# Performance work log

Hardware: AMD Instinct MI355X
Metric: run time of the kernel (lower is better)

The kernel has to match this reference:

```python
import jax, jax.numpy as jnp
import numpy as np

B, D, H = 16384, 64, 128
L = D - 1  # number of per-dimension sub-networks (layers 1..dim-1)
W_SCALE = 0.05  # keep alpha outputs small so exp(alpha) stays well-conditioned


def setup_inputs() -> dict:
    key = jax.random.key(0)
    ks = jax.random.split(key, 8)
    return {
        "x": jax.random.normal(ks[0], (B, D), dtype=jnp.float32),
        "W1": jax.random.normal(ks[1], (L, D - 1, H), dtype=jnp.float32) * W_SCALE,
        "b1": jax.random.normal(ks[2], (L, H), dtype=jnp.float32) * W_SCALE,
        "W2": jax.random.normal(ks[3], (L, H, H), dtype=jnp.float32) * W_SCALE,
        "b2": jax.random.normal(ks[4], (L, H), dtype=jnp.float32) * W_SCALE,
        "W3": jax.random.normal(ks[5], (L, H, 2), dtype=jnp.float32) * W_SCALE,
        "b3": jax.random.normal(ks[6], (L, 2), dtype=jnp.float32) * W_SCALE,
        "initial_param": jax.random.uniform(
            ks[7], (2,), dtype=jnp.float32,
            minval=-np.sqrt(0.5), maxval=np.sqrt(0.5)),
    }


def reference(x, W1, b1, W2, b2, W3, b3, initial_param):
    # x: [B, D]. Layer l (l=0..L-1) corresponds to dim i=l+1 and consumes
    # x[:, :l+1]; we realize the ragged inputs via a triangular mask on W1.
    b, d = x.shape
    # mask[l, j] = 1 if input feature j is visible to layer l (j <= l)
    mask = (jnp.arange(d - 1)[None, :] <= jnp.arange(L)[:, None]).astype(x.dtype)
    W1m = W1 * mask[:, :, None]                       # [L, D-1, H]
    h = jnp.tanh(jnp.einsum('bd,ldh->blh', x[:, :d - 1], W1m) + b1)  # [B, L, H]
    h = jnp.tanh(jnp.einsum('blh,lhk->blk', h, W2) + b2)             # [B, L, H]
    out = jnp.einsum('blh,lho->blo', h, W3) + b3                     # [B, L, 2]
    mu0 = jnp.broadcast_to(initial_param[0], (b, 1))
    a0 = jnp.broadcast_to(initial_param[1], (b, 1))
    mu = jnp.concatenate([mu0, out[..., 0]], axis=1)   # [B, D]
    alpha = jnp.concatenate([a0, out[..., 1]], axis=1)  # [B, D]
    z = (x - mu) * jnp.exp(-alpha)
    log_det = -jnp.sum(alpha, axis=1)                  # [B]
    return z[:, ::-1], log_det
```

## Files before the change

### kernel.cpp

```cpp
#include <hip/hip_runtime.h>
#include <hip/hip_bf16.h>
#include <stdint.h>

#define B_N   16384
#define L_N   63
#define K2LOG2E 2.8853900817779268f
#define LOG2E   1.4426950408889634f

typedef unsigned int   u32;
typedef unsigned short u16;
typedef __attribute__((ext_vector_type(8))) __bf16 bf16x8;
typedef __attribute__((ext_vector_type(4))) float  f32x4;

__device__ __forceinline__ u16 f2b(float f){
  u32 u = __builtin_bit_cast(u32, f);
  u += 0x7fffu + ((u >> 16) & 1u);
  return (u16)(u >> 16);
}
__device__ __forceinline__ u32 pk_bf16(float lo, float hi){
  u32 r;
  asm("v_cvt_pk_bf16_f32 %0, %1, %2" : "=v"(r) : "v"(lo), "v"(hi));
  return r;
}
__device__ __forceinline__ float tanh_pre(float a){
  float t = __builtin_amdgcn_exp2f(a * K2LOG2E);
  float r = __builtin_amdgcn_rcpf(t + 1.0f);
  return fmaf(-2.0f, r, 1.0f);
}
__device__ __forceinline__ float tanh_b(float acc, float bb){
  float t = __builtin_amdgcn_exp2f(fmaf(acc, K2LOG2E, bb));
  float r = __builtin_amdgcn_rcpf(t + 1.0f);
  return fmaf(-2.0f, r, 1.0f);
}

__global__ void k_conv_w(const float* __restrict__ W1, const float* __restrict__ b1,
                         const float* __restrict__ W2,
                         u16* __restrict__ w1t, u16* __restrict__ w2t){
  __shared__ u16 t[16384];
  const int l = blockIdx.x, tid = threadIdx.x;
  #pragma unroll
  for (int i = 0; i < 32; ++i) t[i*256 + tid] = 0;
  __syncthreads();
  for (int i = 0; i < 32; ++i){
    int idx = i*256 + tid;
    if (idx < 63*128){
      int d = idx >> 7, n = idx & 127;
      if (d <= l) t[n*64 + d] = f2b(W1[(l*63 + d)*128 + n]);
    }
  }
  if (tid < 128) t[tid*64 + 63] = f2b(b1[l*128 + tid]);
  __syncthreads();
  {
    uint4* o = (uint4*)(w1t + l*(128*64));
    const uint4* s4 = (const uint4*)t;
    #pragma unroll
    for (int i = 0; i < 4; ++i) o[i*256 + tid] = s4[i*256 + tid];
  }
  __syncthreads();
  #pragma unroll
  for (int i = 0; i < 64; ++i){
    int idx = i*256 + tid;
    int h = idx >> 7, n = idx & 127;
    t[n*128 + h] = f2b(W2[l*16384 + idx]);
  }
  __syncthreads();
  {
    uint4* o = (uint4*)(w2t + l*(128*128));
    const uint4* s4 = (const uint4*)t;
    #pragma unroll
    for (int i = 0; i < 8; ++i) o[i*256 + tid] = s4[i*256 + tid];
  }
}

__global__ void k_conv_x(const float* __restrict__ x, u16* __restrict__ out){
  int idx = blockIdx.x*256 + threadIdx.x;
  float4 v = ((const float4*)x)[idx];
  ushort4 r;
  r.x = f2b(v.x); r.y = f2b(v.y); r.z = f2b(v.z);
  r.w = ((idx & 15) == 15) ? (u16)0x3F80 : f2b(v.w);
  ((ushort4*)out)[idx] = r;
}

__global__ __launch_bounds__(256, 4)
void k_main(const u16* __restrict__ W1T, const u16* __restrict__ W2T,
            const u16* __restrict__ xbf, const float* __restrict__ x,
            const float* __restrict__ b2, const float* __restrict__ W3,
            const float* __restrict__ b3,
            float* __restrict__ out, float* __restrict__ alph)
{
  __shared__ __align__(16) u16 h1[128*128];
  __shared__ float2 sc[4][128];
  const int tid = threadIdx.x;
  const int l  = blockIdx.y;
  const int bx = blockIdx.x;
  const int wv = tid >> 6;
  const int ln = tid & 63;
  const int c  = ln & 15;
  const int g  = ln >> 4;
  const int rowbase = bx*128;
  const int sx = (c & 7) << 4;
  char* const h1b = (char*)h1;

  const u16* w1p = W1T + l*(128*64);
  const u16* w2p = W2T + l*(128*128);

  bf16x8 a1f[2][2];
  #pragma unroll
  for (int m = 0; m < 2; ++m)
    #pragma unroll
    for (int s = 0; s < 2; ++s)
      a1f[m][s] = *(const bf16x8*)(w1p + ((2*wv+m)*16 + c)*64 + s*32 + g*8);

  f32x4 acc[2][8] = {};
  #pragma unroll
  for (int s = 0; s < 2; ++s)
    #pragma unroll
    for (int bt = 0; bt < 8; ++bt){
      bf16x8 xf = *(const bf16x8*)(xbf + (size_t)(rowbase + bt*16 + c)*64 + s*32 + g*8);
      acc[0][bt] = __builtin_amdgcn_mfma_f32_16x16x32_bf16(a1f[0][s], xf, acc[0][bt], 0,0,0);
      acc[1][bt] = __builtin_amdgcn_mfma_f32_16x16x32_bf16(a1f[1][s], xf, acc[1][bt], 0,0,0);
    }

  #pragma unroll
  for (int m = 0; m < 2; ++m){
    int h0 = (2*wv+m)*16 + g*4;
    #pragma unroll
    for (int bt = 0; bt < 8; ++bt){
      u32 p0 = pk_bf16(tanh_pre(acc[m][bt][0]), tanh_pre(acc[m][bt][1]));
      u32 p1 = pk_bf16(tanh_pre(acc[m][bt][2]), tanh_pre(acc[m][bt][3]));
      int b = bt*16 + c;
      *(uint2*)(h1b + b*256 + ((h0*2) ^ sx)) = make_uint2(p0, p1);
    }
  }
  __syncthreads();

  f32x4 acc2[2][8] = {};
  #pragma unroll
  for (int s = 0; s < 4; ++s){
    bf16x8 a0 = *(const bf16x8*)(w2p + ((2*wv+0)*16 + c)*128 + s*32 + g*8);
    bf16x8 a1 = *(const bf16x8*)(w2p + ((2*wv+1)*16 + c)*128 + s*32 + g*8);
    #pragma unroll
    for (int bt = 0; bt < 8; ++bt){
      int b = bt*16 + c;
      bf16x8 hf = *(const bf16x8*)(h1b + b*256 + ((s*64 + g*16) ^ sx));
      acc2[0][bt] = __builtin_amdgcn_mfma_f32_16x16x32_bf16(a0, hf, acc2[0][bt], 0,0,0);
      acc2[1][bt] = __builtin_amdgcn_mfma_f32_16x16x32_bf16(a1, hf, acc2[1][bt], 0,0,0);
    }
  }

  float part[8][2] = {};
  #pragma unroll
  for (int m = 0; m < 2; ++m){
    int q = (2*wv+m)*4 + g;
    float4 bbv = ((const float4*)(b2 + l*128))[q];
    float4 w3a = ((const float4*)(W3 + l*256))[q*2 + 0];
    float4 w3b = ((const float4*)(W3 + l*256))[q*2 + 1];
    float bb[4]  = { bbv.x*K2LOG2E, bbv.y*K2LOG2E, bbv.z*K2LOG2E, bbv.w*K2LOG2E };
    float w30[4] = { w3a.x, w3a.z, w3b.x, w3b.z };
    float w31[4] = { w3a.y, w3a.w, w3b.y, w3b.w };
    #pragma unroll
    for (int bt = 0; bt < 8; ++bt)
      #pragma unroll
      for (int r = 0; r < 4; ++r){
        float h2 = tanh_b(acc2[m][bt][r], bb[r]);
        part[bt][0] = fmaf(h2, w30[r], part[bt][0]);
        part[bt][1] = fmaf(h2, w31[r], part[bt][1]);
      }
  }
  #pragma unroll
  for (int bt = 0; bt < 8; ++bt)
    #pragma unroll
    for (int o = 0; o < 2; ++o){
      float v = part[bt][o];
      v += __shfl_xor(v, 16, 64);
      v += __shfl_xor(v, 32, 64);
      part[bt][o] = v;
    }
  if (g == 0){
    #pragma unroll
    for (int bt = 0; bt < 8; ++bt)
      sc[wv][bt*16 + c] = make_float2(part[bt][0], part[bt][1]);
  }
  __syncthreads();

  if (tid < 128){
    int row = rowbase + tid;
    float2 s0 = sc[0][tid], s1 = sc[1][tid], s2 = sc[2][tid], s3 = sc[3][tid];
    float muv = s0.x + s1.x + s2.x + s3.x + b3[l*2 + 0];
    float alv = s0.y + s1.y + s2.y + s3.y + b3[l*2 + 1];
    float xv  = x[(size_t)row*64 + l + 1];
    out[(size_t)row*64 + 62 - l] = (xv - muv) * __builtin_amdgcn_exp2f(-alv * LOG2E);
    alph[(size_t)row*64 + l + 1] = alv;
  }
}

__global__ void k_fin(const float* __restrict__ x, const float* __restrict__ alph,
                      const float* __restrict__ ip, float* __restrict__ out)
{
  int row = blockIdx.x*4 + (threadIdx.x >> 6);
  int d   = threadIdx.x & 63;
  float a = (d == 0) ? ip[1] : alph[(size_t)row*64 + d];
  float s = a;
  #pragma unroll
  for (int off = 32; off; off >>= 1) s += __shfl_xor(s, off, 64);
  if (d == 0){
    out[(size_t)row*64 + 63] = (x[(size_t)row*64] - ip[0]) * __builtin_amdgcn_exp2f(-a * LOG2E);
    out[(size_t)B_N*64 + row] = -s;
  }
}

extern "C" void kernel_launch(void* const* d_in, const int* in_sizes, int n_in,
                              void* d_out, int out_size, void* d_ws, size_t ws_size,
                              hipStream_t stream)
{
  const float* x  = (const float*)d_in[0];
  const float* W1 = (const float*)d_in[1];
  const float* b1 = (const float*)d_in[2];
  const float* W2 = (const float*)d_in[3];
  const float* b2 = (const float*)d_in[4];
  const float* W3 = (const float*)d_in[5];
  const float* b3 = (const float*)d_in[6];
  const float* ip = (const float*)d_in[7];

  char* ws = (char*)d_ws;
  u16*   w1t  = (u16*)(ws);
  u16*   w2t  = (u16*)(ws + 1048576);
  u16*   xbf  = (u16*)(ws + 3145728);
  float* alph = (float*)(ws + 5242880);
  if (ws_size < 9437184) return;

  k_conv_w<<<L_N, 256, 0, stream>>>(W1, b1, W2, w1t, w2t);
  k_conv_x<<<(B_N*64/4)/256, 256, 0, stream>>>(x, xbf);

  dim3 grid(B_N/128, L_N);
  k_main<<<grid, 256, 0, stream>>>(w1t, w2t, xbf, x, b2, W3, b3,
                                   (float*)d_out, alph);

  k_fin<<<B_N/4, 256, 0, stream>>>(x, alph, ip, (float*)d_out);
}
```

Before: 149.4 us.

## Split main kernel work by batch rows per wave, removing block barriers

Each wave now owns 32 batch rows and computes all 128 hidden units for them, instead of each wave owning 32 hidden units across all 128 rows. The first-layer output stays in a private LDS region per wave, so both __syncthreads and the cross-wave reduction through shared memory go away, and each wave writes its own mu/alpha results. In exchange, every wave loads the full W1 and W2 tiles from global/L2, about four times the weight traffic per block, and the row-level output stores are now spread over lanes with g==0 across waves.

After: 240.9 us. +61.3%, slower.

```diff
diff --git a/kernel.cpp b/kernel.cpp
--- a/kernel.cpp
+++ b/kernel.cpp
@@ -88,8 +88,7 @@
             const float* __restrict__ b3,
             float* __restrict__ out, float* __restrict__ alph)
 {
-  __shared__ __align__(16) u16 h1[128*128];
-  __shared__ float2 sc[4][128];
+  __shared__ __align__(16) char lds[32768];
   const int tid = threadIdx.x;
   const int l  = blockIdx.y;
   const int bx = blockIdx.x;
@@ -97,61 +96,60 @@
   const int ln = tid & 63;
   const int c  = ln & 15;
   const int g  = ln >> 4;
-  const int rowbase = bx*128;
+  const int row0 = bx*128 + wv*32;
+  char* const my = lds + wv*8192;
   const int sx = (c & 7) << 4;
-  char* const h1b = (char*)h1;
 
   const u16* w1p = W1T + l*(128*64);
   const u16* w2p = W2T + l*(128*128);
 
-  bf16x8 a1f[2][2];
-  #pragma unroll
-  for (int m = 0; m < 2; ++m)
+  bf16x8 xf[2][2];
+  #pragma unroll
+  for (int bt = 0; bt < 2; ++bt)
     #pragma unroll
     for (int s = 0; s < 2; ++s)
-      a1f[m][s] = *(const bf16x8*)(w1p + ((2*wv+m)*16 + c)*64 + s*32 + g*8);
-
-  f32x4 acc[2][8] = {};
-  #pragma unroll
-  for (int s = 0; s < 2; ++s)
-    #pragma unroll
-    for (int bt = 0; bt < 8; ++bt){
-      bf16x8 xf = *(const bf16x8*)(xbf + (size_t)(rowbase + bt*16 + c)*64 + s*32 + g*8);
-      acc[0][bt] = __builtin_amdgcn_mfma_f32_16x16x32_bf16(a1f[0][s], xf, acc[0][bt], 0,0,0);
-      acc[1][bt] = __builtin_amdgcn_mfma_f32_16x16x32_bf16(a1f[1][s], xf, acc[1][bt], 0,0,0);
-    }
-
-  #pragma unroll
-  for (int m = 0; m < 2; ++m){
-    int h0 = (2*wv+m)*16 + g*4;
-    #pragma unroll
-    for (int bt = 0; bt < 8; ++bt){
-      u32 p0 = pk_bf16(tanh_pre(acc[m][bt][0]), tanh_pre(acc[m][bt][1]));
-      u32 p1 = pk_bf16(tanh_pre(acc[m][bt][2]), tanh_pre(acc[m][bt][3]));
+      xf[bt][s] = *(const bf16x8*)(xbf + (size_t)(row0 + bt*16 + c)*64 + s*32 + g*8);
+
+  #pragma unroll
+  for (int m = 0; m < 8; ++m){
+    const u16* ap = w1p + (m*16 + c)*64 + g*8;
+    bf16x8 a0 = *(const bf16x8*)(ap);
+    bf16x8 a1 = *(const bf16x8*)(ap + 32);
+    f32x4 acc[2] = {};
+    acc[0] = __builtin_amdgcn_mfma_f32_16x16x32_bf16(a0, xf[0][0], acc[0], 0,0,0);
+    acc[0] = __builtin_amdgcn_mfma_f32_16x16x32_bf16(a1, xf[0][1], acc[0], 0,0,0);
+    acc[1] = __builtin_amdgcn_mfma_f32_16x16x32_bf16(a0, xf[1][0], acc[1], 0,0,0);
+    acc[1] = __builtin_amdgcn_mfma_f32_16x16x32_bf16(a1, xf[1][1], acc[1], 0,0,0);
+    #pragma unroll
+    for (int bt = 0; bt < 2; ++bt){
+      u32 p0 = pk_bf16(tanh_pre(acc[bt][0]), tanh_pre(acc[bt][1]));
+      u32 p1 = pk_bf16(tanh_pre(acc[bt][2]), tanh_pre(acc[bt][3]));
       int b = bt*16 + c;
-      *(uint2*)(h1b + b*256 + ((h0*2) ^ sx)) = make_uint2(p0, p1);
-    }
-  }
-  __syncthreads();
-
-  f32x4 acc2[2][8] = {};
-  #pragma unroll
-  for (int s = 0; s < 4; ++s){
-    bf16x8 a0 = *(const bf16x8*)(w2p + ((2*wv+0)*16 + c)*128 + s*32 + g*8);
-    bf16x8 a1 = *(const bf16x8*)(w2p + ((2*wv+1)*16 + c)*128 + s*32 + g*8);
-    #pragma unroll
-    for (int bt = 0; bt < 8; ++bt){
+      *(uint2*)(my + b*256 + ((m*32 + g*8) ^ sx)) = make_uint2(p0, p1);
+    }
+  }
+
+  bf16x8 hf[4][2];
+  #pragma unroll
+  for (int s = 0; s < 4; ++s)
+    #pragma unroll
+    for (int bt = 0; bt < 2; ++bt){
       int b = bt*16 + c;
-      bf16x8 hf = *(const bf16x8*)(h1b + b*256 + ((s*64 + g*16) ^ sx));
-      acc2[0][bt] = __builtin_amdgcn_mfma_f32_16x16x32_bf16(a0, hf, acc2[0][bt], 0,0,0);
-      acc2[1][bt] = __builtin_amdgcn_mfma_f32_16x16x32_bf16(a1, hf, acc2[1][bt], 0,0,0);
-    }
-  }
-
-  float part[8][2] = {};
-  #pragma unroll
-  for (int m = 0; m < 2; ++m){
-    int q = (2*wv+m)*4 + g;
+      hf[s][bt] = *(const bf16x8*)(my + b*256 + ((s*64 + g*16) ^ sx));
+    }
+
+  float part[2][2] = {};
+  #pragma unroll
+  for (int m = 0; m < 8; ++m){
+    const u16* ap = w2p + (m*16 + c)*128 + g*8;
+    f32x4 acc[2] = {};
+    #pragma unroll
+    for (int s = 0; s < 4; ++s){
+      bf16x8 a = *(const bf16x8*)(ap + s*32);
+      acc[0] = __builtin_amdgcn_mfma_f32_16x16x32_bf16(a, hf[s][0], acc[0], 0,0,0);
+      acc[1] = __builtin_amdgcn_mfma_f32_16x16x32_bf16(a, hf[s][1], acc[1], 0,0,0);
+    }
+    int q = m*4 + g;
     float4 bbv = ((const float4*)(b2 + l*128))[q];
     float4 w3a = ((const float4*)(W3 + l*256))[q*2 + 0];
     float4 w3b = ((const float4*)(W3 + l*256))[q*2 + 1];
@@ -159,16 +157,17 @@
     float w30[4] = { w3a.x, w3a.z, w3b.x, w3b.z };
     float w31[4] = { w3a.y, w3a.w, w3b.y, w3b.w };
     #pragma unroll
-    for (int bt = 0; bt < 8; ++bt)
+    for (int bt = 0; bt < 2; ++bt)
       #pragma unroll
       for (int r = 0; r < 4; ++r){
-        float h2 = tanh_b(acc2[m][bt][r], bb[r]);
+        float h2 = tanh_b(acc[bt][r], bb[r]);
         part[bt][0] = fmaf(h2, w30[r], part[bt][0]);
         part[bt][1] = fmaf(h2, w31[r], part[bt][1]);
       }
   }
-  #pragma unroll
-  for (int bt = 0; bt < 8; ++bt)
+
+  #pragma unroll
+  for (int bt = 0; bt < 2; ++bt)
     #pragma unroll
     for (int o = 0; o < 2; ++o){
       float v = part[bt][o];
@@ -178,19 +177,14 @@
     }
   if (g == 0){
     #pragma unroll
-    for (int bt = 0; bt < 8; ++bt)
-      sc[wv][bt*16 + c] = make_float2(part[bt][0], part[bt][1]);
-  }
-  __syncthreads();
-
-  if (tid < 128){
-    int row = rowbase + tid;
-    float2 s0 = sc[0][tid], s1 = sc[1][tid], s2 = sc[2][tid], s3 = sc[3][tid];
-    float muv = s0.x + s1.x + s2.x + s3.x + b3[l*2 + 0];
-    float alv = s0.y + s1.y + s2.y + s3.y + b3[l*2 + 1];
-    float xv  = x[(size_t)row*64 + l + 1];
-    out[(size_t)row*64 + 62 - l] = (xv - muv) * __builtin_amdgcn_exp2f(-alv * LOG2E);
-    alph[(size_t)row*64 + l + 1] = alv;
+    for (int bt = 0; bt < 2; ++bt){
+      int row = row0 + bt*16 + c;
+      float muv = part[bt][0] + b3[l*2 + 0];
+      float alv = part[bt][1] + b3[l*2 + 1];
+      float xv  = x[(size_t)row*64 + l + 1];
+      out[(size_t)row*64 + 62 - l] = (xv - muv) * __builtin_amdgcn_exp2f(-alv * LOG2E);
+      alph[(size_t)row*64 + l + 1] = alv;
+    }
   }
 }
 
```

## Move third layer to MFMA and fold tanh scale and bias into bf16 weights

Applied to the files above, without the earlier changes.

Pre-scales W1, b1, W2 and b2 by 2*log2(e) during weight conversion so tanh needs no extra multiply, and folds b2 into an extra MFMA k-slice against a constant-one fragment. The third layer (H to 2) is now done with MFMA over h2 written back to shared memory in bf16, replacing the per-lane FMA, shuffle and LDS cross-wave reduction. This adds an extra LDS round trip, two more barriers, one extra weight conversion launch, and bf16 rounding of W3 and h2 at the output layer.

New measurement: 149.9 us. Within noise of the previous version (+0.3%).

```diff
diff --git a/kernel.cpp b/kernel.cpp
--- a/kernel.cpp
+++ b/kernel.cpp
@@ -22,21 +22,15 @@
   asm("v_cvt_pk_bf16_f32 %0, %1, %2" : "=v"(r) : "v"(lo), "v"(hi));
   return r;
 }
-__device__ __forceinline__ float tanh_pre(float a){
-  float t = __builtin_amdgcn_exp2f(a * K2LOG2E);
+__device__ __forceinline__ float tanh_sc(float acc){
+  float t = __builtin_amdgcn_exp2f(acc);
   float r = __builtin_amdgcn_rcpf(t + 1.0f);
   return fmaf(-2.0f, r, 1.0f);
 }
-__device__ __forceinline__ float tanh_b(float acc, float bb){
-  float t = __builtin_amdgcn_exp2f(fmaf(acc, K2LOG2E, bb));
-  float r = __builtin_amdgcn_rcpf(t + 1.0f);
-  return fmaf(-2.0f, r, 1.0f);
-}
-
-__global__ void k_conv_w(const float* __restrict__ W1, const float* __restrict__ b1,
-                         const float* __restrict__ W2,
-                         u16* __restrict__ w1t, u16* __restrict__ w2t){
-  __shared__ u16 t[16384];
+
+__global__ void k_conv_w1(const float* __restrict__ W1, const float* __restrict__ b1,
+                          u16* __restrict__ out){
+  __shared__ u16 t[128*64];
   const int l = blockIdx.x, tid = threadIdx.x;
   #pragma unroll
   for (int i = 0; i < 32; ++i) t[i*256 + tid] = 0;
@@ -45,31 +39,51 @@
     int idx = i*256 + tid;
     if (idx < 63*128){
       int d = idx >> 7, n = idx & 127;
-      if (d <= l) t[n*64 + d] = f2b(W1[(l*63 + d)*128 + n]);
-    }
-  }
-  if (tid < 128) t[tid*64 + 63] = f2b(b1[l*128 + tid]);
-  __syncthreads();
-  {
-    uint4* o = (uint4*)(w1t + l*(128*64));
-    const uint4* s4 = (const uint4*)t;
-    #pragma unroll
-    for (int i = 0; i < 4; ++i) o[i*256 + tid] = s4[i*256 + tid];
-  }
+      if (d <= l) t[n*64 + d] = f2b(W1[(l*63 + d)*128 + n] * K2LOG2E);
+    }
+  }
+  if (tid < 128) t[tid*64 + 63] = f2b(b1[l*128 + tid] * K2LOG2E);
+  __syncthreads();
+  uint4* o = (uint4*)(out + l*(128*64));
+  const uint4* s4 = (const uint4*)t;
+  #pragma unroll
+  for (int i = 0; i < 4; ++i) o[i*256 + tid] = s4[i*256 + tid];
+}
+
+__global__ void k_conv_w2(const float* __restrict__ W2, const float* __restrict__ b2,
+                          u16* __restrict__ out){
+  __shared__ u16 t[128*160];
+  const int l = blockIdx.x, tid = threadIdx.x;
+  #pragma unroll
+  for (int i = 0; i < 80; ++i) t[i*256 + tid] = 0;
   __syncthreads();
   #pragma unroll
   for (int i = 0; i < 64; ++i){
     int idx = i*256 + tid;
     int h = idx >> 7, n = idx & 127;
-    t[n*128 + h] = f2b(W2[l*16384 + idx]);
-  }
-  __syncthreads();
-  {
-    uint4* o = (uint4*)(w2t + l*(128*128));
-    const uint4* s4 = (const uint4*)t;
-    #pragma unroll
-    for (int i = 0; i < 8; ++i) o[i*256 + tid] = s4[i*256 + tid];
-  }
+    t[n*160 + h] = f2b(W2[l*16384 + idx] * K2LOG2E);
+  }
+  if (tid < 128) t[tid*160 + 128] = f2b(b2[l*128 + tid] * K2LOG2E);
+  __syncthreads();
+  uint4* o = (uint4*)(out + l*(128*160));
+  const uint4* s4 = (const uint4*)t;
+  #pragma unroll
+  for (int i = 0; i < 10; ++i) o[i*256 + tid] = s4[i*256 + tid];
+}
+
+__global__ void k_conv_w3(const float* __restrict__ W3, u16* __restrict__ out){
+  __shared__ u16 t[16*128];
+  const int l = blockIdx.x, tid = threadIdx.x;
+  #pragma unroll
+  for (int i = 0; i < 8; ++i) t[i*256 + tid] = 0;
+  __syncthreads();
+  if (tid < 128){
+    t[tid]       = f2b(W3[l*256 + tid*2 + 0]);
+    t[128 + tid] = f2b(W3[l*256 + tid*2 + 1]);
+  }
+  __syncthreads();
+  uint4* o = (uint4*)(out + l*(16*128));
+  o[tid] = ((const uint4*)t)[tid];
 }
 
 __global__ void k_conv_x(const float* __restrict__ x, u16* __restrict__ out){
@@ -83,13 +97,11 @@
 
 __global__ __launch_bounds__(256, 4)
 void k_main(const u16* __restrict__ W1T, const u16* __restrict__ W2T,
-            const u16* __restrict__ xbf, const float* __restrict__ x,
-            const float* __restrict__ b2, const float* __restrict__ W3,
-            const float* __restrict__ b3,
+            const u16* __restrict__ W3T, const u16* __restrict__ xbf,
+            const float* __restrict__ x, const float* __restrict__ b3,
             float* __restrict__ out, float* __restrict__ alph)
 {
-  __shared__ __align__(16) u16 h1[128*128];
-  __shared__ float2 sc[4][128];
+  __shared__ __align__(16) char h1b[128*256];
   const int tid = threadIdx.x;
   const int l  = blockIdx.y;
   const int bx = blockIdx.x;
@@ -99,10 +111,10 @@
   const int g  = ln >> 4;
   const int rowbase = bx*128;
   const int sx = (c & 7) << 4;
-  char* const h1b = (char*)h1;
 
   const u16* w1p = W1T + l*(128*64);
-  const u16* w2p = W2T + l*(128*128);
+  const u16* w2p = W2T + l*(128*160);
+  const u16* w3p = W3T + l*(16*128);
 
   bf16x8 a1f[2][2];
   #pragma unroll
@@ -126,19 +138,22 @@
     int h0 = (2*wv+m)*16 + g*4;
     #pragma unroll
     for (int bt = 0; bt < 8; ++bt){
-      u32 p0 = pk_bf16(tanh_pre(acc[m][bt][0]), tanh_pre(acc[m][bt][1]));
-      u32 p1 = pk_bf16(tanh_pre(acc[m][bt][2]), tanh_pre(acc[m][bt][3]));
+      u32 p0 = pk_bf16(tanh_sc(acc[m][bt][0]), tanh_sc(acc[m][bt][1]));
+      u32 p1 = pk_bf16(tanh_sc(acc[m][bt][2]), tanh_sc(acc[m][bt][3]));
       int b = bt*16 + c;
       *(uint2*)(h1b + b*256 + ((h0*2) ^ sx)) = make_uint2(p0, p1);
     }
   }
   __syncthreads();
 
+  uint4 cw; cw.x = (g == 0) ? 0x00003F80u : 0u; cw.y = cw.z = cw.w = 0u;
+  bf16x8 cf = __builtin_bit_cast(bf16x8, cw);
+
   f32x4 acc2[2][8] = {};
   #pragma unroll
   for (int s = 0; s < 4; ++s){
-    bf16x8 a0 = *(const bf16x8*)(w2p + ((2*wv+0)*16 + c)*128 + s*32 + g*8);
-    bf16x8 a1 = *(const bf16x8*)(w2p + ((2*wv+1)*16 + c)*128 + s*32 + g*8);
+    bf16x8 a0 = *(const bf16x8*)(w2p + ((2*wv+0)*16 + c)*160 + s*32 + g*8);
+    bf16x8 a1 = *(const bf16x8*)(w2p + ((2*wv+1)*16 + c)*160 + s*32 + g*8);
     #pragma unroll
     for (int bt = 0; bt < 8; ++bt){
       int b = bt*16 + c;
@@ -147,50 +162,64 @@
       acc2[1][bt] = __builtin_amdgcn_mfma_f32_16x16x32_bf16(a1, hf, acc2[1][bt], 0,0,0);
     }
   }
-
-  float part[8][2] = {};
+  {
+    bf16x8 ab0 = *(const bf16x8*)(w2p + ((2*wv+0)*16 + c)*160 + 128 + g*8);
+    bf16x8 ab1 = *(const bf16x8*)(w2p + ((2*wv+1)*16 + c)*160 + 128 + g*8);
+    #pragma unroll
+    for (int bt = 0; bt < 8; ++bt){
+      acc2[0][bt] = __builtin_amdgcn_mfma_f32_16x16x32_bf16(ab0, cf, acc2[0][bt], 0,0,0);
+      acc2[1][bt] = __builtin_amdgcn_mfma_f32_16x16x32_bf16(ab1, cf, acc2[1][bt], 0,0,0);
+    }
+  }
+
+  uint2 u2h[2][8];
+  #pragma unroll
+  for (int m = 0; m < 2; ++m)
+    #pragma unroll
+    for (int bt = 0; bt < 8; ++bt){
+      u32 p0 = pk_bf16(tanh_sc(acc2[m][bt][0]), tanh_sc(acc2[m][bt][1]));
+      u32 p1 = pk_bf16(tanh_sc(acc2[m][bt][2]), tanh_sc(acc2[m][bt][3]));
+      u2h[m][bt] = make_uint2(p0, p1);
+    }
+  __syncthreads();
   #pragma unroll
   for (int m = 0; m < 2; ++m){
-    int q = (2*wv+m)*4 + g;
-    float4 bbv = ((const float4*)(b2 + l*128))[q];
-    float4 w3a = ((const float4*)(W3 + l*256))[q*2 + 0];
-    float4 w3b = ((const float4*)(W3 + l*256))[q*2 + 1];
-    float bb[4]  = { bbv.x*K2LOG2E, bbv.y*K2LOG2E, bbv.z*K2LOG2E, bbv.w*K2LOG2E };
-    float w30[4] = { w3a.x, w3a.z, w3b.x, w3b.z };
-    float w31[4] = { w3a.y, w3a.w, w3b.y, w3b.w };
-    #pragma unroll
-    for (int bt = 0; bt < 8; ++bt)
-      #pragma unroll
-      for (int r = 0; r < 4; ++r){
-        float h2 = tanh_b(acc2[m][bt][r], bb[r]);
-        part[bt][0] = fmaf(h2, w30[r], part[bt][0]);
-        part[bt][1] = fmaf(h2, w31[r], part[bt][1]);
-      }
-  }
-  #pragma unroll
-  for (int bt = 0; bt < 8; ++bt)
-    #pragma unroll
-    for (int o = 0; o < 2; ++o){
-      float v = part[bt][o];
-      v += __shfl_xor(v, 16, 64);
-      v += __shfl_xor(v, 32, 64);
-      part[bt][o] = v;
-    }
+    int n0 = (2*wv+m)*16 + g*4;
+    #pragma unroll
+    for (int bt = 0; bt < 8; ++bt){
+      int b = bt*16 + c;
+      *(uint2*)(h1b + b*256 + ((n0*2) ^ sx)) = u2h[m][bt];
+    }
+  }
+  __syncthreads();
+
+  bf16x8 a3[4];
+  #pragma unroll
+  for (int s = 0; s < 4; ++s)
+    a3[s] = *(const bf16x8*)(w3p + c*128 + s*32 + g*8);
+
+  f32x4 acc3[2] = {};
+  #pragma unroll
+  for (int bt = 0; bt < 2; ++bt){
+    int b = (2*wv + bt)*16 + c;
+    #pragma unroll
+    for (int s = 0; s < 4; ++s){
+      bf16x8 hb = *(const bf16x8*)(h1b + b*256 + ((s*64 + g*16) ^ sx));
+      acc3[bt] = __builtin_amdgcn_mfma_f32_16x16x32_bf16(a3[s], hb, acc3[bt], 0,0,0);
+    }
+  }
+
   if (g == 0){
-    #pragma unroll
-    for (int bt = 0; bt < 8; ++bt)
-      sc[wv][bt*16 + c] = make_float2(part[bt][0], part[bt][1]);
-  }
-  __syncthreads();
-
-  if (tid < 128){
-    int row = rowbase + tid;
-    float2 s0 = sc[0][tid], s1 = sc[1][tid], s2 = sc[2][tid], s3 = sc[3][tid];
-    float muv = s0.x + s1.x + s2.x + s3.x + b3[l*2 + 0];
-    float alv = s0.y + s1.y + s2.y + s3.y + b3[l*2 + 1];
-    float xv  = x[(size_t)row*64 + l + 1];
-    out[(size_t)row*64 + 62 - l] = (xv - muv) * __builtin_amdgcn_exp2f(-alv * LOG2E);
-    alph[(size_t)row*64 + l + 1] = alv;
+    float b30 = b3[l*2 + 0], b31 = b3[l*2 + 1];
+    #pragma unroll
+    for (int bt = 0; bt < 2; ++bt){
+      int row = rowbase + (2*wv + bt)*16 + c;
+      float muv = acc3[bt][0] + b30;
+      float alv = acc3[bt][1] + b31;
+      float xv  = x[(size_t)row*64 + l + 1];
+      out[(size_t)row*64 + 62 - l] = (xv - muv) * __builtin_amdgcn_exp2f(-alv * LOG2E);
+      alph[(size_t)row*64 + l + 1] = alv;
+    }
   }
 }
 
@@ -225,15 +254,18 @@
   char* ws = (char*)d_ws;
   u16*   w1t  = (u16*)(ws);
   u16*   w2t  = (u16*)(ws + 1048576);
-  u16*   xbf  = (u16*)(ws + 3145728);
-  float* alph = (float*)(ws + 5242880);
-  if (ws_size < 9437184) return;
-
-  k_conv_w<<<L_N, 256, 0, stream>>>(W1, b1, W2, w1t, w2t);
+  u16*   w3t  = (u16*)(ws + 3670016);
+  u16*   xbf  = (u16*)(ws + 3932160);
+  float* alph = (float*)(ws + 6029312);
+  if (ws_size < 10223616) return;
+
+  k_conv_w1<<<L_N, 256, 0, stream>>>(W1, b1, w1t);
+  k_conv_w2<<<L_N, 256, 0, stream>>>(W2, b2, w2t);
+  k_conv_w3<<<L_N, 256, 0, stream>>>(W3, w3t);
   k_conv_x<<<(B_N*64/4)/256, 256, 0, stream>>>(x, xbf);
 
   dim3 grid(B_N/128, L_N);
-  k_main<<<grid, 256, 0, stream>>>(w1t, w2t, xbf, x, b2, W3, b3,
+  k_main<<<grid, 256, 0, stream>>>(w1t, w2t, w3t, xbf, x, b3,
                                    (float*)d_out, alph);
 
   k_fin<<<B_N/4, 256, 0, stream>>>(x, alph, ip, (float*)d_out);
```

## Fold tanh scale and b2 bias into weights, merge prep kernels

Applied to the files above, without the earlier changes.

The two preprocessing kernels become one launch that also pre-scales W1, b1, W2 and b2 by 2·log2(e), so each tanh skips a multiply or FMA. b2 is stored as an extra padded column of the transposed W2 and added through one more MFMA per tile against a constant one-hot operand, in place of a scalar bias add. W2 fragments and W3 values are loaded earlier, partly before the barrier, so their latency overlaps the layer-1 tanh. The costs are a larger W2 workspace, extra MFMAs, more live registers, and extra bf16 rounding of the bias and scaled weights.

Measured after the change: 133.3 us (median of 2 runs). 10.7% less time.

```diff
diff --git a/kernel.cpp b/kernel.cpp
--- a/kernel.cpp
+++ b/kernel.cpp
@@ -22,22 +22,29 @@
   asm("v_cvt_pk_bf16_f32 %0, %1, %2" : "=v"(r) : "v"(lo), "v"(hi));
   return r;
 }
-__device__ __forceinline__ float tanh_pre(float a){
-  float t = __builtin_amdgcn_exp2f(a * K2LOG2E);
+__device__ __forceinline__ float tanh_sc(float acc){
+  float t = __builtin_amdgcn_exp2f(acc);
   float r = __builtin_amdgcn_rcpf(t + 1.0f);
   return fmaf(-2.0f, r, 1.0f);
 }
-__device__ __forceinline__ float tanh_b(float acc, float bb){
-  float t = __builtin_amdgcn_exp2f(fmaf(acc, K2LOG2E, bb));
-  float r = __builtin_amdgcn_rcpf(t + 1.0f);
-  return fmaf(-2.0f, r, 1.0f);
-}
-
-__global__ void k_conv_w(const float* __restrict__ W1, const float* __restrict__ b1,
-                         const float* __restrict__ W2,
-                         u16* __restrict__ w1t, u16* __restrict__ w2t){
-  __shared__ u16 t[16384];
-  const int l = blockIdx.x, tid = threadIdx.x;
+
+__global__ void k_prep(const float* __restrict__ W1, const float* __restrict__ b1,
+                       const float* __restrict__ W2, const float* __restrict__ b2,
+                       const float* __restrict__ x,
+                       u16* __restrict__ w1t, u16* __restrict__ w2t,
+                       u16* __restrict__ xbf){
+  const int bid = blockIdx.x, tid = threadIdx.x;
+  if (bid >= L_N){
+    int idx = (bid - L_N)*256 + tid;
+    float4 v = ((const float4*)x)[idx];
+    ushort4 r;
+    r.x = f2b(v.x); r.y = f2b(v.y); r.z = f2b(v.z);
+    r.w = ((idx & 15) == 15) ? (u16)0x3F80 : f2b(v.w);
+    ((ushort4*)xbf)[idx] = r;
+    return;
+  }
+  __shared__ u16 t[128*160];
+  const int l = bid;
   #pragma unroll
   for (int i = 0; i < 32; ++i) t[i*256 + tid] = 0;
   __syncthreads();
@@ -45,10 +52,10 @@
     int idx = i*256 + tid;
     if (idx < 63*128){
       int d = idx >> 7, n = idx & 127;
-      if (d <= l) t[n*64 + d] = f2b(W1[(l*63 + d)*128 + n]);
-    }
-  }
-  if (tid < 128) t[tid*64 + 63] = f2b(b1[l*128 + tid]);
+      if (d <= l) t[n*64 + d] = f2b(W1[(l*63 + d)*128 + n] * K2LOG2E);
+    }
+  }
+  if (tid < 128) t[tid*64 + 63] = f2b(b1[l*128 + tid] * K2LOG2E);
   __syncthreads();
   {
     uint4* o = (uint4*)(w1t + l*(128*64));
@@ -58,34 +65,28 @@
   }
   __syncthreads();
   #pragma unroll
+  for (int i = 0; i < 80; ++i) t[i*256 + tid] = 0;
+  __syncthreads();
+  #pragma unroll
   for (int i = 0; i < 64; ++i){
     int idx = i*256 + tid;
     int h = idx >> 7, n = idx & 127;
-    t[n*128 + h] = f2b(W2[l*16384 + idx]);
-  }
+    t[n*160 + h] = f2b(W2[l*16384 + idx] * K2LOG2E);
+  }
+  if (tid < 128) t[tid*160 + 128] = f2b(b2[l*128 + tid] * K2LOG2E);
   __syncthreads();
   {
-    uint4* o = (uint4*)(w2t + l*(128*128));
+    uint4* o = (uint4*)(w2t + l*(128*160));
     const uint4* s4 = (const uint4*)t;
     #pragma unroll
-    for (int i = 0; i < 8; ++i) o[i*256 + tid] = s4[i*256 + tid];
-  }
-}
-
-__global__ void k_conv_x(const float* __restrict__ x, u16* __restrict__ out){
-  int idx = blockIdx.x*256 + threadIdx.x;
-  float4 v = ((const float4*)x)[idx];
-  ushort4 r;
-  r.x = f2b(v.x); r.y = f2b(v.y); r.z = f2b(v.z);
-  r.w = ((idx & 15) == 15) ? (u16)0x3F80 : f2b(v.w);
-  ((ushort4*)out)[idx] = r;
+    for (int i = 0; i < 10; ++i) o[i*256 + tid] = s4[i*256 + tid];
+  }
 }
 
 __global__ __launch_bounds__(256, 4)
 void k_main(const u16* __restrict__ W1T, const u16* __restrict__ W2T,
             const u16* __restrict__ xbf, const float* __restrict__ x,
-            const float* __restrict__ b2, const float* __restrict__ W3,
-            const float* __restrict__ b3,
+            const float* __restrict__ W3, const float* __restrict__ b3,
             float* __restrict__ out, float* __restrict__ alph)
 {
   __shared__ __align__(16) u16 h1[128*128];
@@ -102,7 +103,7 @@
   char* const h1b = (char*)h1;
 
   const u16* w1p = W1T + l*(128*64);
-  const u16* w2p = W2T + l*(128*128);
+  const u16* w2p = W2T + l*(128*160);
 
   bf16x8 a1f[2][2];
   #pragma unroll
@@ -121,61 +122,82 @@
       acc[1][bt] = __builtin_amdgcn_mfma_f32_16x16x32_bf16(a1f[1][s], xf, acc[1][bt], 0,0,0);
     }
 
+  bf16x8 a2[2][4];
+  #pragma unroll
+  for (int m = 0; m < 2; ++m)
+    #pragma unroll
+    for (int s = 0; s < 2; ++s)
+      a2[m][s] = *(const bf16x8*)(w2p + ((2*wv+m)*16 + c)*160 + s*32 + g*8);
+  float w30[2][4], w31[2][4];
+  #pragma unroll
+  for (int m = 0; m < 2; ++m){
+    int q = (2*wv+m)*4 + g;
+    float4 w3a = ((const float4*)(W3 + l*256))[q*2 + 0];
+    float4 w3b = ((const float4*)(W3 + l*256))[q*2 + 1];
+    w30[m][0]=w3a.x; w30[m][1]=w3a.z; w30[m][2]=w3b.x; w30[m][3]=w3b.z;
+    w31[m][0]=w3a.y; w31[m][1]=w3a.w; w31[m][2]=w3b.y; w31[m][3]=w3b.w;
+  }
+
   #pragma unroll
   for (int m = 0; m < 2; ++m){
     int h0 = (2*wv+m)*16 + g*4;
     #pragma unroll
     for (int bt = 0; bt < 8; ++bt){
-      u32 p0 = pk_bf16(tanh_pre(acc[m][bt][0]), tanh_pre(acc[m][bt][1]));
-      u32 p1 = pk_bf16(tanh_pre(acc[m][bt][2]), tanh_pre(acc[m][bt][3]));
+      u32 p0 = pk_bf16(tanh_sc(acc[m][bt][0]), tanh_sc(acc[m][bt][1]));
+      u32 p1 = pk_bf16(tanh_sc(acc[m][bt][2]), tanh_sc(acc[m][bt][3]));
       int b = bt*16 + c;
       *(uint2*)(h1b + b*256 + ((h0*2) ^ sx)) = make_uint2(p0, p1);
     }
   }
   __syncthreads();
 
+  #pragma unroll
+  for (int m = 0; m < 2; ++m)
+    #pragma unroll
+    for (int s = 2; s < 4; ++s)
+      a2[m][s] = *(const bf16x8*)(w2p + ((2*wv+m)*16 + c)*160 + s*32 + g*8);
+  bf16x8 ab[2];
+  #pragma unroll
+  for (int m = 0; m < 2; ++m)
+    ab[m] = *(const bf16x8*)(w2p + ((2*wv+m)*16 + c)*160 + 128 + g*8);
+  uint4 cw; cw.x = (g == 0) ? 0x00003F80u : 0u; cw.y = cw.z = cw.w = 0u;
+  const bf16x8 cf = __builtin_bit_cast(bf16x8, cw);
+
   f32x4 acc2[2][8] = {};
   #pragma unroll
   for (int s = 0; s < 4; ++s){
-    bf16x8 a0 = *(const bf16x8*)(w2p + ((2*wv+0)*16 + c)*128 + s*32 + g*8);
-    bf16x8 a1 = *(const bf16x8*)(w2p + ((2*wv+1)*16 + c)*128 + s*32 + g*8);
     #pragma unroll
     for (int bt = 0; bt < 8; ++bt){
       int b = bt*16 + c;
       bf16x8 hf = *(const bf16x8*)(h1b + b*256 + ((s*64 + g*16) ^ sx));
-      acc2[0][bt] = __builtin_amdgcn_mfma_f32_16x16x32_bf16(a0, hf, acc2[0][bt], 0,0,0);
-      acc2[1][bt] = __builtin_amdgcn_mfma_f32_16x16x32_bf16(a1, hf, acc2[1][bt], 0,0,0);
-    }
+      acc2[0][bt] = __builtin_amdgcn_mfma_f32_16x16x32_bf16(a2[0][s], hf, acc2[0][bt], 0,0,0);
+      acc2[1][bt] = __builtin_amdgcn_mfma_f32_16x16x32_bf16(a2[1][s], hf, acc2[1][bt], 0,0,0);
+    }
+  }
+  #pragma unroll
+  for (int bt = 0; bt < 8; ++bt){
+    acc2[0][bt] = __builtin_amdgcn_mfma_f32_16x16x32_bf16(ab[0], cf, acc2[0][bt], 0,0,0);
+    acc2[1][bt] = __builtin_amdgcn_mfma_f32_16x16x32_bf16(ab[1], cf, acc2[1][bt], 0,0,0);
   }
 
   float part[8][2] = {};
   #pragma unroll
-  for (int m = 0; m < 2; ++m){
-    int q = (2*wv+m)*4 + g;
-    float4 bbv = ((const float4*)(b2 + l*128))[q];
-    float4 w3a = ((const float4*)(W3 + l*256))[q*2 + 0];
-    float4 w3b = ((const float4*)(W3 + l*256))[q*2 + 1];
-    float bb[4]  = { bbv.x*K2LOG2E, bbv.y*K2LOG2E, bbv.z*K2LOG2E, bbv.w*K2LOG2E };
-    float w30[4] = { w3a.x, w3a.z, w3b.x, w3b.z };
-    float w31[4] = { w3a.y, w3a.w, w3b.y, w3b.w };
+  for (int m = 0; m < 2; ++m)
     #pragma unroll
     for (int bt = 0; bt < 8; ++bt)
       #pragma unroll
       for (int r = 0; r < 4; ++r){
-        float h2 = tanh_b(acc2[m][bt][r], bb[r]);
-        part[bt][0] = fmaf(h2, w30[r], part[bt][0]);
-        part[bt][1] = fmaf(h2, w31[r], part[bt][1]);
+        float h2 = tanh_sc(acc2[m][bt][r]);
+        part[bt][0] = fmaf(h2, w30[m][r], part[bt][0]);
+        part[bt][1] = fmaf(h2, w31[m][r], part[bt][1]);
       }
-  }
-  #pragma unroll
-  for (int bt = 0; bt < 8; ++bt)
-    #pragma unroll
-    for (int o = 0; o < 2; ++o){
-      float v = part[bt][o];
-      v += __shfl_xor(v, 16, 64);
-      v += __shfl_xor(v, 32, 64);
-      part[bt][o] = v;
-    }
+  #pragma unroll
+  for (int bt = 0; bt < 8; ++bt){
+    float v0 = part[bt][0], v1 = part[bt][1];
+    v0 += __shfl_xor(v0, 16, 64); v0 += __shfl_xor(v0, 32, 64);
+    v1 += __shfl_xor(v1, 16, 64); v1 += __shfl_xor(v1, 32, 64);
+    part[bt][0] = v0; part[bt][1] = v1;
+  }
   if (g == 0){
     #pragma unroll
     for (int bt = 0; bt < 8; ++bt)
@@ -225,15 +247,15 @@
   char* ws = (char*)d_ws;
   u16*   w1t  = (u16*)(ws);
   u16*   w2t  = (u16*)(ws + 1048576);
-  u16*   xbf  = (u16*)(ws + 3145728);
-  float* alph = (float*)(ws + 5242880);
-  if (ws_size < 9437184) return;
-
-  k_conv_w<<<L_N, 256, 0, stream>>>(W1, b1, W2, w1t, w2t);
-  k_conv_x<<<(B_N*64/4)/256, 256, 0, stream>>>(x, xbf);
+  u16*   xbf  = (u16*)(ws + 3670016);
+  float* alph = (float*)(ws + 5767168);
+  if (ws_size < 9961472) return;
+
+  k_prep<<<L_N + (B_N*64/4)/256, 256, 0, stream>>>(W1, b1, W2, b2, x,
+                                                   w1t, w2t, xbf);
 
   dim3 grid(B_N/128, L_N);
-  k_main<<<grid, 256, 0, stream>>>(w1t, w2t, xbf, x, b2, W3, b3,
+  k_main<<<grid, 256, 0, stream>>>(w1t, w2t, xbf, x, W3, b3,
                                    (float*)d_out, alph);
 
   k_fin<<<B_N/4, 256, 0, stream>>>(x, alph, ip, (float*)d_out);
```
